# Performance work log

Hardware: AMD Instinct MI355X
Metric: run time of the kernel (lower is better)

The kernel has to match this reference:

```python
import jax, jax.numpy as jnp
import numpy as np

FEAT = 64
OUT_DIM = 64
INV_SQRT2 = 0.7071067811865476  # Haar cA of a length-1 zero-padded signal is x/sqrt(2)


def setup_inputs() -> dict:
    key = jax.random.key(0)
    k1, k2, k3, k4, k5, k6 = jax.random.split(key, 6)
    batch, node = 4, 8192
    x = jax.random.normal(k1, (batch, node, FEAT), dtype=jnp.float32)
    adj = jax.random.uniform(k2, (node, node), dtype=jnp.float32) / node  # row-normalized-ish dense adjacency
    # per-feature Linear(wave_len=1 -> 1): weight (feat,), bias (feat,)
    nl_w = jax.random.normal(k3, (FEAT,), dtype=jnp.float32)
    nl_b = jax.random.normal(k4, (FEAT,), dtype=jnp.float32) * 0.01
    # linear_out: (out_dim, feat) weight, (out_dim,) bias
    w_out = jax.random.normal(k5, (OUT_DIM, FEAT), dtype=jnp.float32) / np.sqrt(FEAT)
    b_out = jax.random.normal(k6, (OUT_DIM,), dtype=jnp.float32) * 0.01
    return {"x": x, "adj": adj, "nl_w": nl_w, "nl_b": nl_b, "w_out": w_out, "b_out": b_out}


def reference(x, adj, nl_w, nl_b, w_out, b_out):
    # agg[b,i,f] = sum_j adj[i,j] x[b,j,f]
    agg = jnp.einsum('ij,bjf->bif', adj, x)
    # Haar DWT (J=1, zero mode) of each scalar treated as a length-1 signal -> cA = agg/sqrt(2);
    # per-feature Linear(1->1) then acts elementwise across the feature axis.
    agg_nl = agg * (INV_SQRT2 * nl_w) + nl_b  # (batch, node, feat)
    # linear_out over feature dim; dropout is identity in eval mode
    out = jnp.einsum('bnf,of->bno', agg_nl, w_out) + b_out
    return out
```

## Files before the change

kernel.cpp:

```cpp
#include <hip/hip_runtime.h>

#define NODE 8192
#define FEAT 64
#define OUTD 64
#define NCOL 256

typedef float f32x4 __attribute__((ext_vector_type(4)));
typedef short s16x8 __attribute__((ext_vector_type(8)));
typedef short s16x4 __attribute__((ext_vector_type(4)));
typedef int   i32x4 __attribute__((ext_vector_type(4)));

__device__ __forceinline__ short f2bf(float f) {
    unsigned u = __builtin_bit_cast(unsigned, f);
    u += 0x7FFFu + ((u >> 16) & 1u);
    return (short)(u >> 16);
}

__device__ __forceinline__ s16x4 cvt4(const f32x4& v) {
    s16x4 r;
#pragma unroll
    for (int i = 0; i < 4; ++i) r[i] = f2bf(v[i]);
    return r;
}

__global__ void bias2_kernel(const float* __restrict__ nl_b,
                             const float* __restrict__ w_out,
                             const float* __restrict__ b_out,
                             float* __restrict__ bias2) {
    __shared__ float part[4][64];
    const int o = threadIdx.x & 63;
    const int fc = threadIdx.x >> 6;
    float s = 0.f;
#pragma unroll
    for (int i = 0; i < 16; ++i) {
        int f = fc * 16 + i;
        s += nl_b[f] * w_out[o * FEAT + f];
    }
    part[fc][o] = s;
    __syncthreads();
    if (fc == 0)
        bias2[o] = b_out[o] + part[0][o] + part[1][o] + part[2][o] + part[3][o];
}

__global__ __launch_bounds__(256) void init_out_kernel(
    float* __restrict__ out, const float* __restrict__ bias2) {
    const int idx = (int)blockIdx.x * 256 + threadIdx.x;
    f32x4 bv = *(const f32x4*)(bias2 + ((idx & 15) << 2));
    *(f32x4*)(out + (size_t)idx * 4) = bv;
}

__global__ __launch_bounds__(256) void build_ybf_kernel(
    const float* __restrict__ x, const float* __restrict__ nl_w,
    const float* __restrict__ w_out, unsigned short* __restrict__ ybf) {
    __shared__ float xs[128 * 65];
    __shared__ float w2t[64 * 68];
    const int tid = threadIdx.x;
    const int b   = (int)blockIdx.x >> 6;
    const int j0  = ((int)blockIdx.x & 63) << 7;

    const f32x4* src = (const f32x4*)(x + ((size_t)b * NODE + j0) * FEAT);
#pragma unroll
    for (int it = 0; it < 8; ++it) {
        int i = tid + it * 256;
        f32x4 v = src[i];
        int jl = i >> 4, f0 = (i & 15) << 2;
        float* d = &xs[jl * 65 + f0];
        d[0] = v[0]; d[1] = v[1]; d[2] = v[2]; d[3] = v[3];
    }
#pragma unroll
    for (int it = 0; it < 16; ++it) {
        int i = tid + it * 256;
        int o = i >> 6, f = i & 63;
        w2t[f * 68 + o] = w_out[i] * (0.70710678118654752f * nl_w[f]);
    }
    __syncthreads();

    const int oq = tid & 15;
    const int J  = tid >> 4;
    const float* xr = &xs[(J * 8) * 65];
    const float* wr = &w2t[oq * 4];

    float acc[4][8];
#pragma unroll
    for (int i = 0; i < 4; ++i)
#pragma unroll
        for (int e = 0; e < 8; ++e) acc[i][e] = 0.f;

#pragma unroll 4
    for (int f = 0; f < 64; ++f) {
        f32x4 w4 = *(const f32x4*)(wr + f * 68);
        float xv[8];
#pragma unroll
        for (int e = 0; e < 8; ++e) xv[e] = xr[e * 65 + f];
#pragma unroll
        for (int i = 0; i < 4; ++i)
#pragma unroll
            for (int e = 0; e < 8; ++e) acc[i][e] += w4[i] * xv[e];
    }

    const int jn0 = j0 + J * 8;
    const int kb  = jn0 >> 5;
    const int q   = (jn0 >> 3) & 3;
    const int c16 = b * 4 + (oq >> 2);
    unsigned short* dst = ybf + ((size_t)(c16 * 256 + kb) * 512) +
                          q * 128 + ((oq & 3) * 4) * 8;
#pragma unroll
    for (int i = 0; i < 4; ++i) {
        s16x8 pv;
#pragma unroll
        for (int e = 0; e < 8; ++e) pv[e] = f2bf(acc[i][e]);
        *(s16x8*)(dst + i * 8) = pv;
    }
}

__global__ __launch_bounds__(256, 2) void gemm_adj_kernel(
    const float* __restrict__ adj, const unsigned short* __restrict__ ybf,
    float* __restrict__ out) {
    __shared__ __align__(16) unsigned short As[4][4][32 * 40];

    const int tid  = threadIdx.x;
    const int lane = tid & 63;
    const int wv   = tid >> 6;
    const int bi   = (int)blockIdx.x;
    const int xcd  = bi & 7;
    const int seq  = bi >> 3;
    const int rg   = (seq >> 4) * 8 + xcd;
    const int cg   = (seq >> 2) & 3;
    const int ks   = seq & 3;
    const int row0 = rg * 128 + wv * 32;
    const int t16  = lane & 15;
    const int quad = lane >> 4;
    const int sr   = lane >> 2;
    const int sc   = lane & 3;

    const float* aGr[2];
    aGr[0] = adj + (size_t)(row0 + sr) * NODE + ks * 2048 + sc * 4;
    aGr[1] = aGr[0] + (size_t)16 * NODE;

    const unsigned short* bpB[4];
#pragma unroll
    for (int nt = 0; nt < 4; ++nt)
        bpB[nt] = ybf + ((size_t)((cg * 4 + nt) * 256 + ks * 64) * 512) + lane * 8;

    unsigned short* Aw = &As[wv][0][0];
    const int woff = sr * 40 + sc * 4;

    f32x4 acc[2][4];
#pragma unroll
    for (int mi = 0; mi < 2; ++mi)
#pragma unroll
        for (int nt = 0; nt < 4; ++nt) acc[mi][nt] = (f32x4){0.f, 0.f, 0.f, 0.f};

    f32x4 aR[4][4];
    i32x4 BF[2][4];

#pragma unroll
    for (int s = 0; s < 4; ++s)
#pragma unroll
        for (int g = 0; g < 2; ++g)
#pragma unroll
            for (int j = 0; j < 2; ++j)
                aR[s][g * 2 + j] = *(const f32x4*)(aGr[g] + s * 32 + j * 16);
#pragma unroll
    for (int nt = 0; nt < 4; ++nt) BF[0][nt] = *(const i32x4*)bpB[nt];
#pragma unroll
    for (int s = 0; s < 2; ++s) {
        unsigned short* wb = Aw + s * 1280;
#pragma unroll
        for (int g = 0; g < 2; ++g)
#pragma unroll
            for (int j = 0; j < 2; ++j)
                *(s16x4*)(wb + g * 640 + j * 16 + woff) = cvt4(aR[s][g * 2 + j]);
#pragma unroll
        for (int g = 0; g < 2; ++g)
#pragma unroll
            for (int j = 0; j < 2; ++j)
                aR[s][g * 2 + j] = *(const f32x4*)(aGr[g] + (4 + s) * 32 + j * 16);
    }

#define ROUND(qv, PH)                                                         \
    {                                                                         \
                                                    \
        const int tB = (qv + 1) & 63;                                         \
        _Pragma("unroll") for (int nt = 0; nt < 4; ++nt)                      \
            BF[(PH + 1) & 1][nt] = *(const i32x4*)(bpB[nt] + (size_t)tB * 512); \
                           \
        {                                                                     \
            unsigned short* wb = Aw + ((PH + 2) & 3) * 1280;                  \
            _Pragma("unroll") for (int g = 0; g < 2; ++g)                     \
                _Pragma("unroll") for (int j = 0; j < 2; ++j)                 \
                    *(s16x4*)(wb + g * 640 + j * 16 + woff) =                 \
                        cvt4(aR[(PH + 2) & 3][g * 2 + j]);                    \
        }                                                                     \
                                 \
        {                                                                     \
            const int ko = ((qv + 6) & 63) * 32;                              \
            _Pragma("unroll") for (int g = 0; g < 2; ++g)                     \
                _Pragma("unroll") for (int j = 0; j < 2; ++j)                 \
                    aR[(PH + 2) & 3][g * 2 + j] =                             \
                        *(const f32x4*)(aGr[g] + ko + j * 16);                \
        }                                                                     \
                                                          \
        {                                                                     \
            const unsigned short* rb = Aw + (PH & 3) * 1280;                  \
            s16x8 af0 = *(const s16x8*)(rb + t16 * 40 + quad * 8);            \
            s16x8 af1 = *(const s16x8*)(rb + (16 + t16) * 40 + quad * 8);     \
            _Pragma("unroll") for (int nt = 0; nt < 4; ++nt) {                \
                s16x8 bf = __builtin_bit_cast(s16x8, BF[PH & 1][nt]);         \
                acc[0][nt] = __builtin_amdgcn_mfma_f32_16x16x32_bf16(         \
                    af0, bf, acc[0][nt], 0, 0, 0);                            \
                acc[1][nt] = __builtin_amdgcn_mfma_f32_16x16x32_bf16(         \
                    af1, bf, acc[1][nt], 0, 0, 0);                            \
            }                                                                 \
        }                                                                     \
    }

#pragma unroll 1
    for (int q = 0; q < 64; q += 4) {
        ROUND(q + 0, 0)
        ROUND(q + 1, 1)
        ROUND(q + 2, 2)
        ROUND(q + 3, 3)
    }
#undef ROUND

#pragma unroll
    for (int mi = 0; mi < 2; ++mi) {
        const int i0 = row0 + mi * 16 + quad * 4;
#pragma unroll
        for (int nt = 0; nt < 4; ++nt) {
            float* op = out + ((size_t)cg * NODE + i0) * OUTD + nt * 16 + t16;
#pragma unroll
            for (int rr = 0; rr < 4; ++rr)
                atomicAdd(op + (size_t)rr * OUTD, acc[mi][nt][rr]);
        }
    }
}

extern "C" void kernel_launch(void* const* d_in, const int* in_sizes, int n_in,
                              void* d_out, int out_size, void* d_ws, size_t ws_size,
                              hipStream_t stream) {
    const float* x     = (const float*)d_in[0];
    const float* adj   = (const float*)d_in[1];
    const float* nl_w  = (const float*)d_in[2];
    const float* nl_b  = (const float*)d_in[3];
    const float* w_out = (const float*)d_in[4];
    const float* b_out = (const float*)d_in[5];
    float* out = (float*)d_out;

    unsigned short* ybf = (unsigned short*)d_ws;
    float* bias2 = (float*)((char*)d_ws + (size_t)NCOL * NODE * 2);

    bias2_kernel<<<1, 256, 0, stream>>>(nl_b, w_out, b_out, bias2);
    init_out_kernel<<<2048, 256, 0, stream>>>(out, bias2);
    build_ybf_kernel<<<256, 256, 0, stream>>>(x, nl_w, w_out, ybf);
    gemm_adj_kernel<<<1024, 256, 0, stream>>>(adj, ybf, out);
}
```

Before: 455.8 us.

## Stream fp32 adj tiles directly into LDS and double split-K

The GEMM over the fp32 adjacency now uses global_load_lds to copy tiles straight into shared memory in fp32, with an XOR swizzle. Conversion to bf16 moves to after the LDS read, so registers no longer stage the loads and there is no convert-then-write step. Split-K doubles from 4 to 8 slices, giving 2048 blocks, and the pipeline is managed with explicit vmcnt waits and sched barriers. In exchange, LDS use doubles because tiles are stored in fp32, and there are twice as many atomic adds into the output.

Measured after the change: 467.1 us. +2.5%, slower.

```diff
diff --git a/kernel.cpp b/kernel.cpp
--- a/kernel.cpp
+++ b/kernel.cpp
@@ -16,11 +16,19 @@
     return (short)(u >> 16);
 }
 
-__device__ __forceinline__ s16x4 cvt4(const f32x4& v) {
-    s16x4 r;
-#pragma unroll
-    for (int i = 0; i < 4; ++i) r[i] = f2bf(v[i]);
+__device__ __forceinline__ s16x8 pack8(const f32x4& a, const f32x4& b) {
+    s16x8 r;
+#pragma unroll
+    for (int i = 0; i < 4; ++i) r[i] = f2bf(a[i]);
+#pragma unroll
+    for (int i = 0; i < 4; ++i) r[4 + i] = f2bf(b[i]);
     return r;
+}
+
+__device__ __forceinline__ void gl2lds16(const float* g, float* l) {
+    __builtin_amdgcn_global_load_lds(
+        (const __attribute__((address_space(1))) void*)g,
+        (__attribute__((address_space(3))) void*)l, 16, 0, 0);
 }
 
 __global__ void bias2_kernel(const float* __restrict__ nl_b,
@@ -116,113 +124,101 @@
 __global__ __launch_bounds__(256, 2) void gemm_adj_kernel(
     const float* __restrict__ adj, const unsigned short* __restrict__ ybf,
     float* __restrict__ out) {
-    __shared__ __align__(16) unsigned short As[4][4][32 * 40];
+    __shared__ __align__(16) float As[4][4][1024];
 
     const int tid  = threadIdx.x;
     const int lane = tid & 63;
     const int wv   = tid >> 6;
     const int bi   = (int)blockIdx.x;
     const int xcd  = bi & 7;
-    const int seq  = bi >> 3;
-    const int rg   = (seq >> 4) * 8 + xcd;
-    const int cg   = (seq >> 2) & 3;
-    const int ks   = seq & 3;
+    const int w    = bi >> 3;
+    const int cg   = w & 3;
+    const int ks   = (w >> 2) & 7;
+    const int rg   = (w >> 5) * 8 + xcd;
     const int row0 = rg * 128 + wv * 32;
     const int t16  = lane & 15;
     const int quad = lane >> 4;
-    const int sr   = lane >> 2;
-    const int sc   = lane & 3;
-
-    const float* aGr[2];
-    aGr[0] = adj + (size_t)(row0 + sr) * NODE + ks * 2048 + sc * 4;
-    aGr[1] = aGr[0] + (size_t)16 * NODE;
+
+    const float* aSrc[4];
+#pragma unroll
+    for (int g = 0; g < 4; ++g)
+        aSrc[g] = adj + (size_t)(row0 + g * 8 + (lane >> 3)) * NODE +
+                  ks * 1024 + 4 * ((lane & 7) ^ (lane >> 3));
+
+    int aIdx[2][2];
+#pragma unroll
+    for (int m = 0; m < 2; ++m)
+#pragma unroll
+        for (int h = 0; h < 2; ++h)
+            aIdx[m][h] = (m * 16 + t16) * 32 +
+                         (((quad * 2 + h) ^ (lane & 7)) << 2);
 
     const unsigned short* bpB[4];
 #pragma unroll
     for (int nt = 0; nt < 4; ++nt)
-        bpB[nt] = ybf + ((size_t)((cg * 4 + nt) * 256 + ks * 64) * 512) + lane * 8;
-
-    unsigned short* Aw = &As[wv][0][0];
-    const int woff = sr * 40 + sc * 4;
-
+        bpB[nt] = ybf + ((size_t)((cg * 4 + nt) * 256 + ks * 32) * 512) + lane * 8;
+
+    i32x4 BF[2][4];
     f32x4 acc[2][4];
 #pragma unroll
     for (int mi = 0; mi < 2; ++mi)
 #pragma unroll
         for (int nt = 0; nt < 4; ++nt) acc[mi][nt] = (f32x4){0.f, 0.f, 0.f, 0.f};
 
-    f32x4 aR[4][4];
-    i32x4 BF[2][4];
-
 #pragma unroll
     for (int s = 0; s < 4; ++s)
 #pragma unroll
-        for (int g = 0; g < 2; ++g)
-#pragma unroll
-            for (int j = 0; j < 2; ++j)
-                aR[s][g * 2 + j] = *(const f32x4*)(aGr[g] + s * 32 + j * 16);
+        for (int g = 0; g < 4; ++g)
+            gl2lds16(aSrc[g] + s * 32, &As[wv][s][g * 256]);
+    __builtin_amdgcn_sched_barrier(0);
 #pragma unroll
     for (int nt = 0; nt < 4; ++nt) BF[0][nt] = *(const i32x4*)bpB[nt];
 #pragma unroll
-    for (int s = 0; s < 2; ++s) {
-        unsigned short* wb = Aw + s * 1280;
-#pragma unroll
-        for (int g = 0; g < 2; ++g)
-#pragma unroll
-            for (int j = 0; j < 2; ++j)
-                *(s16x4*)(wb + g * 640 + j * 16 + woff) = cvt4(aR[s][g * 2 + j]);
-#pragma unroll
-        for (int g = 0; g < 2; ++g)
-#pragma unroll
-            for (int j = 0; j < 2; ++j)
-                aR[s][g * 2 + j] = *(const f32x4*)(aGr[g] + (4 + s) * 32 + j * 16);
-    }
-
-#define ROUND(qv, PH)                                                         \
+    for (int nt = 0; nt < 4; ++nt) BF[1][nt] = *(const i32x4*)(bpB[nt] + 512);
+
+#define ROUND(qv, PH, BP)                                                     \
     {                                                                         \
-                                                    \
-        const int tB = (qv + 1) & 63;                                         \
-        _Pragma("unroll") for (int nt = 0; nt < 4; ++nt)                      \
-            BF[(PH + 1) & 1][nt] = *(const i32x4*)(bpB[nt] + (size_t)tB * 512); \
-                           \
+        asm volatile("s_waitcnt vmcnt(12)" ::: "memory");                     \
+        __builtin_amdgcn_sched_barrier(0);                                    \
+        const float* sb = &As[wv][PH][0];                                     \
+        f32x4 a00 = *(const f32x4*)(sb + aIdx[0][0]);                         \
+        f32x4 a01 = *(const f32x4*)(sb + aIdx[0][1]);                         \
+        f32x4 a10 = *(const f32x4*)(sb + aIdx[1][0]);                         \
+        f32x4 a11 = *(const f32x4*)(sb + aIdx[1][1]);                         \
+        s16x8 af0 = pack8(a00, a01);                                          \
+        s16x8 af1 = pack8(a10, a11);                                          \
+        _Pragma("unroll") for (int nt = 0; nt < 4; ++nt) {                    \
+            s16x8 bf = __builtin_bit_cast(s16x8, BF[BP][nt]);                 \
+            acc[0][nt] = __builtin_amdgcn_mfma_f32_16x16x32_bf16(             \
+                af0, bf, acc[0][nt], 0, 0, 0);                                \
+            acc[1][nt] = __builtin_amdgcn_mfma_f32_16x16x32_bf16(             \
+                af1, bf, acc[1][nt], 0, 0, 0);                                \
+        }                                                                     \
         {                                                                     \
-            unsigned short* wb = Aw + ((PH + 2) & 3) * 1280;                  \
-            _Pragma("unroll") for (int g = 0; g < 2; ++g)                     \
-                _Pragma("unroll") for (int j = 0; j < 2; ++j)                 \
-                    *(s16x4*)(wb + g * 640 + j * 16 + woff) =                 \
-                        cvt4(aR[(PH + 2) & 3][g * 2 + j]);                    \
+            const int tB = ((qv) + 2) & 31;                                   \
+            _Pragma("unroll") for (int nt = 0; nt < 4; ++nt)                  \
+                BF[BP][nt] = *(const i32x4*)(bpB[nt] + (size_t)tB * 512);     \
         }                                                                     \
-                                 \
+        __builtin_amdgcn_sched_barrier(0);                                    \
         {                                                                     \
-            const int ko = ((qv + 6) & 63) * 32;                              \
-            _Pragma("unroll") for (int g = 0; g < 2; ++g)                     \
-                _Pragma("unroll") for (int j = 0; j < 2; ++j)                 \
-                    aR[(PH + 2) & 3][g * 2 + j] =                             \
-                        *(const f32x4*)(aGr[g] + ko + j * 16);                \
+            const int tA = ((qv) + 4) & 31;                                   \
+            _Pragma("unroll") for (int g = 0; g < 4; ++g)                     \
+                gl2lds16(aSrc[g] + tA * 32, &As[wv][PH][g * 256]);            \
         }                                                                     \
-                                                          \
-        {                                                                     \
-            const unsigned short* rb = Aw + (PH & 3) * 1280;                  \
-            s16x8 af0 = *(const s16x8*)(rb + t16 * 40 + quad * 8);            \
-            s16x8 af1 = *(const s16x8*)(rb + (16 + t16) * 40 + quad * 8);     \
-            _Pragma("unroll") for (int nt = 0; nt < 4; ++nt) {                \
-                s16x8 bf = __builtin_bit_cast(s16x8, BF[PH & 1][nt]);         \
-                acc[0][nt] = __builtin_amdgcn_mfma_f32_16x16x32_bf16(         \
-                    af0, bf, acc[0][nt], 0, 0, 0);                            \
-                acc[1][nt] = __builtin_amdgcn_mfma_f32_16x16x32_bf16(         \
-                    af1, bf, acc[1][nt], 0, 0, 0);                            \
-            }                                                                 \
-        }                                                                     \
+        __builtin_amdgcn_sched_barrier(0);                                    \
     }
 
 #pragma unroll 1
-    for (int q = 0; q < 64; q += 4) {
-        ROUND(q + 0, 0)
-        ROUND(q + 1, 1)
-        ROUND(q + 2, 2)
-        ROUND(q + 3, 3)
+    for (int q = 0; q < 32; q += 4) {
+        ROUND(q + 0, 0, 0)
+        ROUND(q + 1, 1, 1)
+        ROUND(q + 2, 2, 0)
+        ROUND(q + 3, 3, 1)
     }
 #undef ROUND
+
+    asm volatile("s_waitcnt vmcnt(0)" ::: "memory");
+    __builtin_amdgcn_sched_barrier(0);
 
 #pragma unroll
     for (int mi = 0; mi < 2; ++mi) {
@@ -254,5 +250,5 @@
     bias2_kernel<<<1, 256, 0, stream>>>(nl_b, w_out, b_out, bias2);
     init_out_kernel<<<2048, 256, 0, stream>>>(out, bias2);
     build_ybf_kernel<<<256, 256, 0, stream>>>(x, nl_w, w_out, ybf);
-    gemm_adj_kernel<<<1024, 256, 0, stream>>>(adj, ybf, out);
-}
+    gemm_adj_kernel<<<2048, 256, 0, stream>>>(adj, ybf, out);
+}
```
